# Kernel tuning notes

Hardware: AMD Instinct MI355X
Metric: run time of the kernel (lower is better)

Reference implementation:

```python
import jax, jax.numpy as jnp
import numpy as np
from math import comb

B = 1024                 # num_batch
NUM, NVAR, NUM_OBS = 100, 11, 10
T_FIN = 15.0
K_P = 20.0; K_D = 2.0 * np.sqrt(20.0); K_P_V = 20.0
A_OBS, B_OBS = 8.0, 4.2
RHO_V, RHO_PROJ, RHO_LANE, RHO_OBS, RHO_OFFSET, RHO_INEQ = 1.0, 1.0, 100.0, 100.0, 1.0, 100.0
V_MIN, V_MAX, A_MAX = 0.1, 30.0, 8.0
MAXITER = 20
LATENT, HID, INP_DIM, TRAJ_DIM = 2, 1024, 55, 200


def _bernstein():
    # degree-10 Bernstein polynomial basis on [0, T_FIN], sampled at NUM points
    n = NVAR - 1
    s = np.linspace(0.0, 1.0, NUM)
    bm = lambda m: np.stack([comb(m, k) * s**k * (1.0 - s)**(m - k) for k in range(m + 1)], 1)
    P, B9, B8 = bm(n), bm(n - 1), bm(n - 2)
    Z = np.zeros(NUM)
    Pdot = np.stack([(n / T_FIN) * ((B9[:, k - 1] if k >= 1 else Z) - (B9[:, k] if k <= n - 1 else Z)) for k in range(n + 1)], 1)
    Pddot = np.stack([(n * (n - 1) / T_FIN**2) * ((B8[:, k - 2] if k >= 2 else Z) - 2.0 * (B8[:, k - 1] if 1 <= k <= n - 1 else Z) + (B8[:, k] if k <= n - 2 else Z)) for k in range(n + 1)], 1)
    return tuple(jnp.asarray(a, jnp.float32) for a in (P, Pdot, Pddot))


def _forward(inp, initial_state_ego, traj_gt, y_ub, y_lb, eps,
             enc_w1, enc_b1, enc_w2, enc_b2, enc_wmu, enc_bmu, enc_wlv, enc_blv,
             dec_w1, dec_b1, dec_w2, dec_b2, dec_w3, dec_b3,
             P, Pdot, Pddot, inp_mean, inp_std):
    Bn = inp.shape[0]
    tot_time = jnp.linspace(0.0, T_FIN, NUM)

    # ---- cVAE encode / reparameterize / decode ----
    inp_n = (inp - inp_mean) / inp_std
    h = jax.nn.relu(jnp.concatenate([inp_n, traj_gt], 1) @ enc_w1 + enc_b1)
    h = jax.nn.relu(h @ enc_w2 + enc_b2)
    mu = h @ enc_wmu + enc_bmu
    logvar = h @ enc_wlv + enc_blv
    z = mu + jnp.exp(0.5 * logvar) * eps
    h = jax.nn.relu(jnp.concatenate([z, inp_n], 1) @ dec_w1 + dec_b1)
    h = jax.nn.relu(h @ dec_w2 + dec_b2)
    nn_out = h @ dec_w3 + dec_b3          # (B, 8): 4 v_des + 4 y_des setpoints

    # ---- constant constraint matrices ----
    A_eq_x = jnp.stack([P[0], Pdot[0], Pddot[0]])                 # (3, 11)
    A_eq_y = jnp.stack([P[0], Pdot[0], Pddot[0], Pdot[-1]])       # (4, 11)
    A_pd = Pddot - K_P * P - K_D * Pdot
    A_vd = Pddot - K_P_V * Pdot
    cost_smooth = Pddot.T @ Pddot
    I = jnp.eye(NVAR, dtype=P.dtype)

    def kkt_inv(cost, A_eq):
        m = A_eq.shape[0]
        M = jnp.block([[cost, A_eq.T], [A_eq, jnp.zeros((m, m), cost.dtype)]])
        return jnp.linalg.inv(M)

    # ---- boundary conditions ----
    zb = jnp.zeros((Bn,), inp.dtype)
    b_eq_x = jnp.stack([zb, initial_state_ego[:, 2], zb], 1)
    b_eq_y = jnp.stack([zb, initial_state_ego[:, 3], zb, zb], 1)

    # ---- QP layer 1 (behavioral layer) ----
    # sum_i A_vd_i^T A_vd_i over the 4 row-partitions == A_vd^T A_vd
    cost1_x = cost_smooth + RHO_V * (A_vd.T @ A_vd)
    cost1_y = cost_smooth + RHO_OFFSET * (A_pd.T @ A_pd)
    inv1_x = kkt_inv(cost1_x, A_eq_x)
    inv1_y = kkt_inv(cost1_y, A_eq_y)
    v_des = jnp.repeat(nn_out[:, 0:4], NUM // 4, axis=1)   # (B, 100) piecewise setpoints
    y_des = jnp.repeat(nn_out[:, 4:8], NUM // 4, axis=1)
    lincost_x1 = -RHO_V * ((-K_P_V * v_des) @ A_vd)
    lincost_y1 = -RHO_OFFSET * ((-K_P * y_des) @ A_pd)
    c_x_bar = (jnp.concatenate([-lincost_x1, b_eq_x], 1) @ inv1_x.T)[:, :NVAR]
    c_y_bar = (jnp.concatenate([-lincost_y1, b_eq_y], 1) @ inv1_y.T)[:, :NVAR]

    # ---- obstacle constant-velocity rollouts (obstacle-major, matches tile(P)) ----
    x_obs, y_obs = inp[:, 5::5], inp[:, 6::5]
    vx_obs, vy_obs = inp[:, 7::5], inp[:, 8::5]
    x_obs_traj = (x_obs[:, :, None] + vx_obs[:, :, None] * tot_time).reshape(Bn, NUM_OBS * NUM)
    y_obs_traj = (y_obs[:, :, None] + vy_obs[:, :, None] * tot_time).reshape(Bn, NUM_OBS * NUM)

    # ---- QP layer 2 (iterative ADMM-style projection) ----
    A_obs_m = jnp.tile(P, (NUM_OBS, 1))          # (1000, 11)
    A_lane = jnp.vstack([P, -P])                 # (200, 11)
    A_vel, A_acc = Pdot, Pddot
    cost2_x = RHO_PROJ * I + RHO_OBS * (A_obs_m.T @ A_obs_m) + RHO_INEQ * (A_acc.T @ A_acc) + RHO_INEQ * (A_vel.T @ A_vel)
    cost2_y = cost2_x + RHO_LANE * (A_lane.T @ A_lane)
    inv2_x = kkt_inv(cost2_x, A_eq_x)
    inv2_y = kkt_inv(cost2_y, A_eq_y)
    ones_num = jnp.ones((1, NUM), inp.dtype)
    b_lane = jnp.concatenate([y_ub[:, None] * ones_num, -y_lb[:, None] * ones_num], 1)  # (B, 200)

    def step(carry, _):
        primal, lx, ly = carry
        cx, cy = primal[:, :NVAR], primal[:, NVAR:]
        x, xdot, xddot = cx @ P.T, cx @ Pdot.T, cx @ Pddot.T
        y, ydot, yddot = cy @ P.T, cy @ Pdot.T, cy @ Pddot.T
        # obstacle polar decomposition
        wc = jnp.tile(x, (1, NUM_OBS)) - x_obs_traj
        ws = jnp.tile(y, (1, NUM_OBS)) - y_obs_traj
        a_o = jnp.arctan2(A_OBS * ws, B_OBS * wc)
        ca, sa = jnp.cos(a_o), jnp.sin(a_o)
        c1 = RHO_OBS * (A_OBS**2 * ca**2 + B_OBS**2 * sa**2)
        c2 = RHO_OBS * (A_OBS * wc * ca + B_OBS * ws * sa)
        d_o = jnp.maximum(1.0, c2 / c1)
        # velocity / acceleration polar decomposition with box clipping
        a_v = jnp.arctan2(ydot, xdot)
        cv, sv = jnp.cos(a_v), jnp.sin(a_v)
        d_v = jnp.clip(xdot * cv + ydot * sv, V_MIN, V_MAX)
        a_a = jnp.arctan2(yddot, xddot)
        caa, saa = jnp.cos(a_a), jnp.sin(a_a)
        d_a = jnp.clip(xddot * caa + yddot * saa, 0.0, A_MAX)
        # lane slack
        lane_proj = cy @ A_lane.T
        s_lane = jnp.maximum(0.0, b_lane - lane_proj)
        res_lane = lane_proj - b_lane + s_lane
        # residuals -> dual updates
        rxo = wc - A_OBS * d_o * ca
        ryo = ws - B_OBS * d_o * sa
        rvx, rvy = xdot - d_v * cv, ydot - d_v * sv
        rax, ray = xddot - d_a * caa, yddot - d_a * saa
        lx = lx - RHO_OBS * (rxo @ A_obs_m) - RHO_INEQ * (rax @ A_acc) - RHO_INEQ * (rvx @ A_vel)
        ly = ly - RHO_OBS * (ryo @ A_obs_m) - RHO_INEQ * (ray @ A_acc) - RHO_INEQ * (rvy @ A_vel) - RHO_LANE * (res_lane @ A_lane)
        # linear cost + batched KKT solve via precomputed inverse
        b_ox = x_obs_traj + A_OBS * d_o * ca
        b_oy = y_obs_traj + B_OBS * d_o * sa
        lin_x = -lx - RHO_PROJ * c_x_bar - RHO_OBS * (b_ox @ A_obs_m) - RHO_INEQ * ((d_a * caa) @ A_acc) - RHO_INEQ * ((d_v * cv) @ A_vel)
        lin_y = -ly - RHO_PROJ * c_y_bar - RHO_OBS * (b_oy @ A_obs_m) - RHO_INEQ * ((d_a * saa) @ A_acc) - RHO_INEQ * ((d_v * sv) @ A_vel) - RHO_LANE * ((b_lane - s_lane) @ A_lane)
        sx = (jnp.concatenate([-lin_x, b_eq_x], 1) @ inv2_x.T)[:, :NVAR]
        sy = (jnp.concatenate([-lin_y, b_eq_y], 1) @ inv2_y.T)[:, :NVAR]
        return (jnp.concatenate([sx, sy], 1), lx, ly), None

    primal0 = jnp.concatenate([c_x_bar, c_y_bar], 1)
    lam0 = jnp.zeros((Bn, NVAR), inp.dtype)
    (primal, _, _), _ = jax.lax.scan(step, (primal0, lam0, lam0), None, length=MAXITER)
    return primal  # (B, 2*NVAR) projected trajectory coefficients


def setup_inputs() -> dict:
    key = jax.random.key(0)
    ks = jax.random.split(key, 16)
    P, Pdot, Pddot = _bernstein()
    n = lambda k, sh, sc=1.0: sc * jax.random.normal(k, sh, jnp.float32)
    return {
        "inp": n(ks[0], (B, INP_DIM), 5.0),
        "initial_state_ego": jnp.concatenate([jnp.zeros((B, 2), jnp.float32), 10.0 + n(ks[1], (B, 2))], 1),
        "traj_gt": n(ks[2], (B, TRAJ_DIM)),
        "y_ub": jnp.full((B,), 3.5, jnp.float32),
        "y_lb": jnp.full((B,), -3.5, jnp.float32),
        "eps": n(ks[3], (B, LATENT)),
        "enc_w1": n(ks[4], (INP_DIM + TRAJ_DIM, HID), 0.05), "enc_b1": jnp.zeros((HID,), jnp.float32),
        "enc_w2": n(ks[5], (HID, HID), 0.03), "enc_b2": jnp.zeros((HID,), jnp.float32),
        "enc_wmu": n(ks[6], (HID, LATENT), 0.03), "enc_bmu": jnp.zeros((LATENT,), jnp.float32),
        "enc_wlv": n(ks[7], (HID, LATENT), 0.03), "enc_blv": jnp.zeros((LATENT,), jnp.float32),
        "dec_w1": n(ks[8], (LATENT + INP_DIM, HID), 0.05), "dec_b1": jnp.zeros((HID,), jnp.float32),
        "dec_w2": n(ks[9], (HID, HID), 0.03), "dec_b2": jnp.zeros((HID,), jnp.float32),
        "dec_w3": n(ks[10], (HID, 8), 0.03), "dec_b3": jnp.zeros((8,), jnp.float32),
        "P": P, "Pdot": Pdot, "Pddot": Pddot,
        "inp_mean": jnp.zeros((INP_DIM,), jnp.float32),
        "inp_std": jnp.ones((INP_DIM,), jnp.float32),
    }


def reference(inp, initial_state_ego, traj_gt, y_ub, y_lb, eps,
              enc_w1, enc_b1, enc_w2, enc_b2, enc_wmu, enc_bmu, enc_wlv, enc_blv,
              dec_w1, dec_b1, dec_w2, dec_b2, dec_w3, dec_b3,
              P, Pdot, Pddot, inp_mean, inp_std):
    return _forward(inp, initial_state_ego, traj_gt, y_ub, y_lb, eps,
                    enc_w1, enc_b1, enc_w2, enc_b2, enc_wmu, enc_bmu, enc_wlv, enc_blv,
                    dec_w1, dec_b1, dec_w2, dec_b2, dec_w3, dec_b3,
                    P, Pdot, Pddot, inp_mean, inp_std)
```

## Files before the change

kernel.cpp:

```cpp
#include <hip/hip_runtime.h>
#include <hip/hip_bf16.h>
#include <math.h>

#define BATCH   1024
#define NUMPT   100
#define NVAR    11
#define NOBS    10
#define HID     1024
#define INPD    55
#define TRAJD   200

#define T_FIN_C   15.0f
#define K_P_C     20.0f
#define K_D_C     8.944271909999159f
#define K_P_V_C   20.0f
#define A_OBS_C   8.0f
#define B_OBS_C   4.2f
#define AB_C      33.6f
#define ABSQ_C    1128.96f
#define RHO_V_C      1.0f
#define RHO_PROJ_C   1.0f
#define RHO_LANE_C   100.0f
#define RHO_OBS_C    100.0f
#define RHO_OFFSET_C 1.0f
#define RHO_INEQ_C   100.0f
#define V_MIN_C   0.1f
#define V_MAX_C   30.0f
#define A_MAX_C   8.0f
#define MAXIT     20

#define WS_INV1X  0
#define WS_INV1Y  256
#define WS_INV2X  512
#define WS_INV2Y  768
#define WS_SVD    1024
#define WS_SPD    1088
#define WS_QX     1152
#define WS_QY     1280
#define WS_R2X    1408
#define WS_R2Y    1536
#define WS_BIG    2048

typedef __bf16 bf16x8 __attribute__((ext_vector_type(8)));
typedef float  f32x4  __attribute__((ext_vector_type(4)));

__global__ __launch_bounds__(256) void setup_kernel(
    const float* __restrict__ Pg, const float* __restrict__ Pdg,
    const float* __restrict__ Pddg, float* __restrict__ ws,
    const float* __restrict__ inp, const float* __restrict__ traj,
    const float* __restrict__ mean, const float* __restrict__ stdv,
    __bf16* __restrict__ enc_in, __bf16* __restrict__ dec_in,
    const float* __restrict__ w1, const float* __restrict__ w2,
    const float* __restrict__ w3, const float* __restrict__ w4,
    __bf16* __restrict__ o1, __bf16* __restrict__ o2,
    __bf16* __restrict__ o3, __bf16* __restrict__ o4)
{
    __shared__ float sP[NUMPT*NVAR], sPd[NUMPT*NVAR], sPdd[NUMPT*NVAR];
    __shared__ float aug[15][31];
    __shared__ float fcol[15];
    __shared__ float sQ[121];
    __shared__ float sn[INPD];
    __shared__ float s_pivinv;
    __shared__ int   s_pidx;
    const int tid = threadIdx.x, bid = blockIdx.x;

    if (bid >= 1028) {
        const int idx = (bid - 1028) * 256 + tid;
        if (idx < 262144) {
            const int n = idx >> 8, k = idx & 255;
            o1[idx] = (__bf16)((k < 255) ? w1[(size_t)k*HID + n] : 0.0f);
        } else if (idx < 262144 + 1048576) {
            const int i = idx - 262144;
            const int n = i >> 10, k = i & 1023;
            o2[i] = (__bf16)w2[(size_t)k*HID + n];
        } else if (idx < 262144 + 1048576 + 65536) {
            const int i = idx - (262144 + 1048576);
            const int n = i >> 6, k = i & 63;
            o3[i] = (__bf16)((k < 57) ? w3[(size_t)k*HID + n] : 0.0f);
        } else {
            const int i = idx - (262144 + 1048576 + 65536);
            const int n = i >> 10, k = i & 1023;
            o4[i] = (__bf16)w4[(size_t)k*HID + n];
        }
        return;
    }

    if (bid >= 4) {
        const int b = bid - 4;
        if (tid < INPD) {
            const float v = (inp[b*INPD + tid] - mean[tid]) / stdv[tid];
            sn[tid] = v;
            enc_in[b*256 + tid] = (__bf16)v;
        } else if (tid < 255) {
            enc_in[b*256 + tid] = (__bf16)traj[b*TRAJD + (tid - INPD)];
        } else {
            enc_in[b*256 + 255] = (__bf16)0.0f;
        }
        __syncthreads();
        if (tid >= 2 && tid < 64)
            dec_in[b*64 + tid] = (__bf16)((tid < 57) ? sn[tid - 2] : 0.0f);
        return;
    }

    for (int i = tid; i < NUMPT*NVAR; i += 256) {
        sP[i] = Pg[i]; sPd[i] = Pdg[i]; sPdd[i] = Pddg[i];
    }
    for (int i = tid; i < 15*31; i += 256) (&aug[0][0])[i] = 0.0f;
    __syncthreads();

    const int N = (bid == 0 || bid == 2) ? 14 : 15;

    if (tid < 121) {
        const int i = tid / 11, j = tid % 11;
        float s = 0.0f;
        if (bid == 0) {
            for (int t = 0; t < NUMPT; ++t) {
                float pdd_i = sPdd[t*NVAR+i], pdd_j = sPdd[t*NVAR+j];
                float av_i = pdd_i - K_P_V_C * sPd[t*NVAR+i];
                float av_j = pdd_j - K_P_V_C * sPd[t*NVAR+j];
                s += pdd_i*pdd_j + RHO_V_C * av_i*av_j;
            }
        } else if (bid == 1) {
            for (int t = 0; t < NUMPT; ++t) {
                float pdd_i = sPdd[t*NVAR+i], pdd_j = sPdd[t*NVAR+j];
                float ap_i = pdd_i - K_P_C*sP[t*NVAR+i] - K_D_C*sPd[t*NVAR+i];
                float ap_j = pdd_j - K_P_C*sP[t*NVAR+j] - K_D_C*sPd[t*NVAR+j];
                s += pdd_i*pdd_j + RHO_OFFSET_C * ap_i*ap_j;
            }
        } else {
            float obs_w = RHO_OBS_C * (float)NOBS;
            if (bid == 3) obs_w += RHO_LANE_C * 2.0f;
            for (int t = 0; t < NUMPT; ++t) {
                float p_i = sP[t*NVAR+i],   p_j = sP[t*NVAR+j];
                float pd_i = sPd[t*NVAR+i], pd_j = sPd[t*NVAR+j];
                float pdd_i = sPdd[t*NVAR+i], pdd_j = sPdd[t*NVAR+j];
                s += obs_w*p_i*p_j + RHO_INEQ_C*(pdd_i*pdd_j + pd_i*pd_j);
            }
            if (i == j) s += RHO_PROJ_C;
        }
        aug[i][j] = s;
    }
    if (tid < 11) {
        const int i = tid;
        float a0 = sP[i], a1 = sPd[i], a2 = sPdd[i];
        aug[i][11] = a0; aug[11][i] = a0;
        aug[i][12] = a1; aug[12][i] = a1;
        aug[i][13] = a2; aug[13][i] = a2;
        if (N == 15) { float a3 = sPd[99*NVAR + i]; aug[i][14] = a3; aug[14][i] = a3; }
    }
    if (tid < N) aug[tid][N + tid] = 1.0f;

    if (bid == 0 && tid < 44) {
        const int c = tid / 11, k = tid % 11;
        float sv = 0.0f, sp = 0.0f;
        for (int t = 25*c; t < 25*c + 25; ++t) {
            float p = sP[t*NVAR+k], pd = sPd[t*NVAR+k], pdd = sPdd[t*NVAR+k];
            sv += pdd - K_P_V_C * pd;
            sp += pdd - K_P_C * p - K_D_C * pd;
        }
        ws[WS_SVD + tid] = sv;
        ws[WS_SPD + tid] = sp;
    }
    __syncthreads();

    if ((bid == 2 || bid == 3) && tid < 121) {
        float v = aug[tid/11][tid%11];
        if (tid/11 == tid%11) v -= RHO_PROJ_C;
        sQ[tid] = v;
        ws[(bid == 2 ? WS_QX : WS_QY) + tid] = v;
    }

    for (int k = 0; k < N; ++k) {
        if (tid == 0) {
            int p = k; float best = fabsf(aug[k][k]);
            for (int i = k+1; i < N; ++i) {
                float v = fabsf(aug[i][k]);
                if (v > best) { best = v; p = i; }
            }
            s_pidx = p;
        }
        __syncthreads();
        const int p = s_pidx;
        if (p != k && tid < 2*N) {
            float tmp = aug[k][tid]; aug[k][tid] = aug[p][tid]; aug[p][tid] = tmp;
        }
        __syncthreads();
        if (tid == 0) s_pivinv = 1.0f / aug[k][k];
        __syncthreads();
        if (tid < 2*N) aug[k][tid] *= s_pivinv;
        __syncthreads();
        if (tid < N) fcol[tid] = (tid == k) ? 0.0f : aug[tid][k];
        __syncthreads();
        for (int idx = tid; idx < N*2*N; idx += 256) {
            const int i = idx / (2*N), j = idx % (2*N);
            if (i != k) aug[i][j] = fmaf(-fcol[i], aug[k][j], aug[i][j]);
        }
        __syncthreads();
    }

    float* dst = ws + (bid == 0 ? WS_INV1X : bid == 1 ? WS_INV1Y
                      : bid == 2 ? WS_INV2X : WS_INV2Y);
    for (int idx = tid; idx < N*N; idx += 256)
        dst[idx] = aug[idx / N][N + idx % N];
    __syncthreads();

    if ((bid == 2 || bid == 3) && tid < 121) {
        const int k = tid / 11, j = tid % 11;
        float a = 0.0f;
        #pragma unroll
        for (int m = 0; m < 11; ++m) a = fmaf(aug[k][N + m], sQ[m*11 + j], a);
        ws[(bid == 2 ? WS_R2X : WS_R2Y) + tid] = a;
    }
}

__global__ __launch_bounds__(512) void gemm_mfma(
    const __bf16* __restrict__ A, const __bf16* __restrict__ Wt,
    const float* __restrict__ bias, __bf16* __restrict__ C, int Kp)
{
    __shared__ __bf16 As[64][72];
    __shared__ __bf16 Bs[64][72];
    const int tid = threadIdx.x;
    const int lane = tid & 63, wv = tid >> 6;
    const int wm = (wv >> 1) * 16, wn = (wv & 1) * 32;
    const int ln = lane & 15, q = lane >> 4;
    const int row0 = blockIdx.y * 64, col0 = blockIdx.x * 64;
    const int lrow = tid >> 3, lc = (tid & 7) * 8;

    f32x4 acc0 = (f32x4){0,0,0,0}, acc1 = (f32x4){0,0,0,0};

    for (int k0 = 0; k0 < Kp; k0 += 64) {
        *(bf16x8*)&As[lrow][lc] =
            *(const bf16x8*)&A[(size_t)(row0 + lrow) * Kp + k0 + lc];
        *(bf16x8*)&Bs[lrow][lc] =
            *(const bf16x8*)&Wt[(size_t)(col0 + lrow) * Kp + k0 + lc];
        __syncthreads();
        #pragma unroll
        for (int kc = 0; kc < 2; ++kc) {
            const bf16x8 a  = *(const bf16x8*)&As[wm + ln][kc*32 + q*8];
            const bf16x8 b0 = *(const bf16x8*)&Bs[wn + ln][kc*32 + q*8];
            const bf16x8 b1 = *(const bf16x8*)&Bs[wn + 16 + ln][kc*32 + q*8];
            acc0 = __builtin_amdgcn_mfma_f32_16x16x32_bf16(a, b0, acc0, 0, 0, 0);
            acc1 = __builtin_amdgcn_mfma_f32_16x16x32_bf16(a, b1, acc1, 0, 0, 0);
        }
        __syncthreads();
    }
    #pragma unroll
    for (int ni = 0; ni < 2; ++ni) {
        const int col = col0 + wn + ni*16 + ln;
        const float bv = bias[col];
        const f32x4 av = ni ? acc1 : acc0;
        #pragma unroll
        for (int r = 0; r < 4; ++r) {
            const int row = row0 + wm + q*4 + r;
            C[(size_t)row * HID + col] = (__bf16)fmaxf(av[r] + bv, 0.0f);
        }
    }
}

__global__ __launch_bounds__(64) void z_kernel(
    const __bf16* __restrict__ h, const float* __restrict__ wmu,
    const float* __restrict__ bmu, const float* __restrict__ wlv,
    const float* __restrict__ blv, const float* __restrict__ eps,
    __bf16* __restrict__ dec_in)
{
    const int b = blockIdx.x, lane = threadIdx.x;
    float a0 = 0, a1 = 0, a2 = 0, a3 = 0;
    for (int hh = lane; hh < HID; hh += 64) {
        const float v = (float)h[b*HID + hh];
        a0 = fmaf(v, wmu[hh*2 + 0], a0);
        a1 = fmaf(v, wmu[hh*2 + 1], a1);
        a2 = fmaf(v, wlv[hh*2 + 0], a2);
        a3 = fmaf(v, wlv[hh*2 + 1], a3);
    }
    #pragma unroll
    for (int off = 32; off; off >>= 1) {
        a0 += __shfl_down(a0, off);
        a1 += __shfl_down(a1, off);
        a2 += __shfl_down(a2, off);
        a3 += __shfl_down(a3, off);
    }
    if (lane == 0) {
        const float mu0 = a0 + bmu[0], mu1 = a1 + bmu[1];
        const float lv0 = a2 + blv[0], lv1 = a3 + blv[1];
        dec_in[b*64 + 0] = (__bf16)fmaf(expf(0.5f*lv0), eps[b*2 + 0], mu0);
        dec_in[b*64 + 1] = (__bf16)fmaf(expf(0.5f*lv1), eps[b*2 + 1], mu1);
    }
}

__global__ __launch_bounds__(64) void out8_kernel(
    const __bf16* __restrict__ h, const float* __restrict__ w3,
    const float* __restrict__ b3, float* __restrict__ nn_out)
{
    const int b = blockIdx.x, lane = threadIdx.x;
    float acc[8] = {};
    for (int hh = lane; hh < HID; hh += 64) {
        const float v = (float)h[b*HID + hh];
        #pragma unroll
        for (int j = 0; j < 8; ++j) acc[j] = fmaf(v, w3[hh*8 + j], acc[j]);
    }
    #pragma unroll
    for (int j = 0; j < 8; ++j)
        #pragma unroll
        for (int off = 32; off; off >>= 1) acc[j] += __shfl_down(acc[j], off);
    if (lane == 0)
        for (int j = 0; j < 8; ++j) nn_out[b*8 + j] = acc[j] + b3[j];
}

#define DOT11(bb, a0, a1, a2) \
    fmaf(bb[0],a0.x, fmaf(bb[1],a0.y, fmaf(bb[2],a0.z, fmaf(bb[3],a0.w, \
    fmaf(bb[4],a1.x, fmaf(bb[5],a1.y, fmaf(bb[6],a1.z, fmaf(bb[7],a1.w, \
    fmaf(bb[8],a2.x, fmaf(bb[9],a2.y, bb[10]*a2.z))))))))))

__global__ __launch_bounds__(256) void solver_kernel(
    const float* __restrict__ nn_out, const float* __restrict__ inp,
    const float* __restrict__ ise, const float* __restrict__ yub_p,
    const float* __restrict__ ylb_p,
    const float* __restrict__ Pg, const float* __restrict__ Pdg,
    const float* __restrict__ Pddg,
    const float* __restrict__ ws, float* __restrict__ out)
{
    __shared__ __align__(16) float sBcol[3][11][108];
    __shared__ float s_i2x[196], s_i2y[225], sR2x[121], sR2y[121];
    __shared__ __align__(16) float rows[9][104];
    __shared__ float dval[2][100];
    __shared__ __align__(16) float cxs[12], cys[12];
    __shared__ float wlin[24];
    __shared__ float obsS[4][10];

    const int tid = threadIdx.x;
    const int e = blockIdx.x;

    for (int i = tid; i < 3*11*108; i += 256) {
        const int mat = i / 1188, rem = i - mat*1188;
        const int k = rem / 108, t = rem - k*108;
        const float* G = (mat == 0) ? Pg : (mat == 1 ? Pdg : Pddg);
        sBcol[mat][k][t] = (t < NUMPT) ? G[t*NVAR + k] : 0.0f;
    }
    for (int i = tid; i < 196; i += 256) s_i2x[i] = ws[WS_INV2X + i];
    for (int i = tid; i < 225; i += 256) s_i2y[i] = ws[WS_INV2Y + i];
    for (int i = tid; i < 121; i += 256) { sR2x[i] = ws[WS_R2X + i]; sR2y[i] = ws[WS_R2Y + i]; }
    if (tid >= 200 && tid < 240) {
        const int i = tid - 200;
        obsS[i/10][i%10] = inp[e*INPD + 5 + (i/10) + 5*(i%10)];
    }
    if (tid >= 64 && tid < 100) {
        const int i = tid - 64;
        rows[i >> 2][100 + (i & 3)] = 0.0f;
    }
    if (tid == 100) cxs[11] = 0.0f;
    if (tid == 101) cys[11] = 0.0f;

    const bool isA = (tid < 200);
    const int tA = tid >> 1, hA = tid & 1;
    const bool isB = (tid < 198);
    const int hB = (tid >= 99) ? 1 : 0;
    const int dB = tid - 99*hB;
    const int rB = dB / 11, kB = dB - 11*rB;
    const int mB = (rB==2||rB==6) ? 2 : ((rB==3||rB==7) ? 1 : 0);
    const float* colp = &sBcol[mB][kB][hB*52];
    const float* rowp = &rows[rB][hB*52];

    float bP[NVAR], bPd[NVAR], bPdd[NVAR];
    if (isA) {
        #pragma unroll
        for (int k = 0; k < NVAR; ++k) bP[k] = Pg[tA*NVAR+k];
        if (hA == 0) {
            #pragma unroll
            for (int k = 0; k < NVAR; ++k) {
                bPd[k] = Pdg[tA*NVAR+k]; bPdd[k] = Pddg[tA*NVAR+k];
            }
        }
    }

    const float vx0 = ise[e*4 + 2], vy0 = ise[e*4 + 3];
    const float yub = yub_p[e], ylb = ylb_p[e];
    __syncthreads();

    const float DT = T_FIN_C / 99.0f;
    float xo[5], yo[5];
    if (isA) {
        const int ob0 = 5*hA;
        #pragma unroll
        for (int o = 0; o < 5; ++o) {
            xo[o] = fmaf(obsS[2][ob0+o], tA*DT, obsS[0][ob0+o]);
            yo[o] = fmaf(obsS[3][ob0+o], tA*DT, obsS[1][ob0+o]);
        }
    }

    if (tid < 11) {
        float s = 0;
        #pragma unroll
        for (int c = 0; c < 4; ++c)
            s = fmaf(nn_out[e*8 + c], ws[WS_SVD + c*11 + tid], s);
        wlin[tid] = RHO_V_C * K_P_V_C * s;
    } else if (tid < 22) {
        const int k = tid - 11;
        float s = 0;
        #pragma unroll
        for (int c = 0; c < 4; ++c)
            s = fmaf(nn_out[e*8 + 4 + c], ws[WS_SPD + c*11 + k], s);
        wlin[tid] = RHO_OFFSET_C * K_P_C * s;
    }
    __syncthreads();

    float lam = 0.0f, cb = 0.0f;
    if (tid < 11) {
        const int k = tid;
        float a = vx0 * ws[WS_INV1X + k*14 + 12];
        #pragma unroll
        for (int j = 0; j < NVAR; ++j)
            a = fmaf(-wlin[j], ws[WS_INV1X + k*14 + j], a);
        cb = a; cxs[k] = a;
    } else if (tid < 22) {
        const int k = tid - 11;
        float a = vy0 * ws[WS_INV1Y + k*15 + 12];
        #pragma unroll
        for (int j = 0; j < NVAR; ++j)
            a = fmaf(-wlin[11 + j], ws[WS_INV1Y + k*15 + j], a);
        cb = a; cys[k] = a;
    }
    __syncthreads();

    for (int it = 0; it < MAXIT; ++it) {
        if (isA) {
            const float4 x0 = *(const float4*)&cxs[0];
            const float4 x1 = *(const float4*)&cxs[4];
            const float4 x2 = *(const float4*)&cxs[8];
            const float4 y0 = *(const float4*)&cys[0];
            const float4 y1 = *(const float4*)&cys[4];
            const float4 y2 = *(const float4*)&cys[8];
            const float px = DOT11(bP, x0, x1, x2);
            const float py = DOT11(bP, y0, y1, y2);

            float srx = 0.0f, sry = 0.0f;
            #pragma unroll
            for (int o = 0; o < 5; ++o) {
                const float wc = px - xo[o], wsv = py - yo[o];
                const float aw = A_OBS_C * wsv, bw = B_OBS_C * wc;
                const float r2 = aw*aw + bw*bw;
                if (r2 > 0.0f) {
                    const float f = (r2 < ABSQ_C) ? (1.0f - AB_C * rsqrtf(r2)) : 0.0f;
                    srx = fmaf(wc, f, srx);
                    sry = fmaf(wsv, f, sry);
                } else {
                    srx -= A_OBS_C;
                }
            }
            rows[hA ? 1 : 0][tA] = srx;
            rows[hA ? 5 : 4][tA] = sry;

            if (hA == 0) {
                const float pxd  = DOT11(bPd,  x0, x1, x2);
                const float pyd  = DOT11(bPd,  y0, y1, y2);
                const float pxdd = DOT11(bPdd, x0, x1, x2);
                const float pydd = DOT11(bPdd, y0, y1, y2);
                const float rv2 = pxd*pxd + pyd*pyd;
                float vxr, vyr;
                if (rv2 > 0.0f) {
                    const float ri = rsqrtf(rv2);
                    const float dv = fminf(fmaxf(rv2*ri, V_MIN_C), V_MAX_C);
                    const float f = 1.0f - dv*ri;
                    vxr = pxd*f; vyr = pyd*f;
                } else { vxr = -V_MIN_C; vyr = 0.0f; }
                rows[3][tA] = vxr;  rows[7][tA] = vyr;
                const float ra2 = pxdd*pxdd + pydd*pydd;
                float axr = 0.0f, ayr = 0.0f;
                if (ra2 > ABSQ_C*0.0f + A_MAX_C*A_MAX_C) {
                    const float ri = rsqrtf(ra2);
                    const float f = 1.0f - A_MAX_C*ri;
                    axr = pxdd*f; ayr = pydd*f;
                }
                rows[2][tA] = axr;  rows[6][tA] = ayr;
                rows[8][tA] = fmaxf(0.0f, py - yub) - fmaxf(0.0f, ylb - py);
            }
        }
        __syncthreads();

        if (isB) {
            float s = 0.0f;
            #pragma unroll
            for (int i = 0; i < 13; ++i) {
                const float4 rr = *(const float4*)&rowp[i*4];
                const float4 cc = *(const float4*)&colp[i*4];
                s = fmaf(rr.x, cc.x, s); s = fmaf(rr.y, cc.y, s);
                s = fmaf(rr.z, cc.z, s); s = fmaf(rr.w, cc.w, s);
            }
            dval[hB][dB] = s;
        }
        __syncthreads();

        if (tid < 22) {
            const int k = (tid < 11) ? tid : tid - 11;
            float u;
            if (tid < 11)
                u = RHO_OBS_C * ((dval[0][k]      + dval[1][k])
                               + (dval[0][11 + k] + dval[1][11 + k])
                               + (dval[0][22 + k] + dval[1][22 + k])
                               + (dval[0][33 + k] + dval[1][33 + k]));
            else
                u = RHO_OBS_C * ((dval[0][44 + k] + dval[1][44 + k])
                               + (dval[0][55 + k] + dval[1][55 + k])
                               + (dval[0][66 + k] + dval[1][66 + k])
                               + (dval[0][77 + k] + dval[1][77 + k])
                               + (dval[0][88 + k] + dval[1][88 + k]));
            wlin[tid] = 2.0f*u - lam - cb;
            lam -= u;
        }
        __builtin_amdgcn_wave_barrier();
        if (tid < 22) {
            const int k = (tid < 11) ? tid : tid - 11;
            if (tid < 11) {
                float a = vx0 * s_i2x[k*14 + 12];
                #pragma unroll
                for (int j = 0; j < NVAR; ++j) {
                    a = fmaf(-wlin[j], s_i2x[k*14 + j], a);
                    a = fmaf(sR2x[k*11 + j], cxs[j], a);
                }
                cxs[k] = a;
            } else {
                float a = vy0 * s_i2y[k*15 + 12];
                #pragma unroll
                for (int j = 0; j < NVAR; ++j) {
                    a = fmaf(-wlin[11 + j], s_i2y[k*15 + j], a);
                    a = fmaf(sR2y[k*11 + j], cys[j], a);
                }
                cys[k] = a;
            }
        }
        __syncthreads();
    }

    if (tid < NVAR) {
        out[e*22 + tid]      = cxs[tid];
        out[e*22 + 11 + tid] = cys[tid];
    }
}

extern "C" void kernel_launch(void* const* d_in, const int* in_sizes, int n_in,
                              void* d_out, int out_size, void* d_ws, size_t ws_size,
                              hipStream_t stream)
{
    (void)in_sizes; (void)n_in; (void)out_size; (void)ws_size;
    const float* inp    = (const float*)d_in[0];
    const float* ise    = (const float*)d_in[1];
    const float* traj   = (const float*)d_in[2];
    const float* yub    = (const float*)d_in[3];
    const float* ylb    = (const float*)d_in[4];
    const float* eps    = (const float*)d_in[5];
    const float* enc_w1 = (const float*)d_in[6];
    const float* enc_b1 = (const float*)d_in[7];
    const float* enc_w2 = (const float*)d_in[8];
    const float* enc_b2 = (const float*)d_in[9];
    const float* wmu    = (const float*)d_in[10];
    const float* bmu    = (const float*)d_in[11];
    const float* wlv    = (const float*)d_in[12];
    const float* blv    = (const float*)d_in[13];
    const float* dec_w1 = (const float*)d_in[14];
    const float* dec_b1 = (const float*)d_in[15];
    const float* dec_w2 = (const float*)d_in[16];
    const float* dec_b2 = (const float*)d_in[17];
    const float* dec_w3 = (const float*)d_in[18];
    const float* dec_b3 = (const float*)d_in[19];
    const float* P      = (const float*)d_in[20];
    const float* Pd     = (const float*)d_in[21];
    const float* Pdd    = (const float*)d_in[22];
    const float* mean   = (const float*)d_in[23];
    const float* stdv   = (const float*)d_in[24];

    float* ws   = (float*)d_ws;
    float* nn   = ws + WS_BIG;
    __bf16* bfb = (__bf16*)(ws + WS_BIG + BATCH*8);
    __bf16* enc_in = bfb;
    __bf16* dec_in = enc_in + (size_t)BATCH*256;
    __bf16* hA     = dec_in + (size_t)BATCH*64;
    __bf16* hB     = hA + (size_t)BATCH*HID;
    __bf16* wt1    = hB + (size_t)BATCH*HID;
    __bf16* wt2    = wt1 + (size_t)HID*256;
    __bf16* wt3    = wt2 + (size_t)HID*HID;
    __bf16* wt4    = wt3 + (size_t)HID*64;
    float* outf = (float*)d_out;

    setup_kernel<<<4 + 1024 + 9472, 256, 0, stream>>>(
        P, Pd, Pdd, ws, inp, traj, mean, stdv, enc_in, dec_in,
        enc_w1, enc_w2, dec_w1, dec_w2, wt1, wt2, wt3, wt4);

    dim3 g(16, 16);
    gemm_mfma<<<g, 512, 0, stream>>>(enc_in, wt1, enc_b1, hA, 256);
    gemm_mfma<<<g, 512, 0, stream>>>(hA, wt2, enc_b2, hB, 1024);
    z_kernel<<<BATCH, 64, 0, stream>>>(hB, wmu, bmu, wlv, blv, eps, dec_in);
    gemm_mfma<<<g, 512, 0, stream>>>(dec_in, wt3, dec_b1, hA, 64);
    gemm_mfma<<<g, 512, 0, stream>>>(hA, wt4, dec_b2, hB, 1024);
    out8_kernel<<<BATCH, 64, 0, stream>>>(hB, dec_w3, dec_b3, nn);

    solver_kernel<<<BATCH, 256, 0, stream>>>(nn, inp, ise, yub, ylb,
                                             P, Pd, Pdd, ws, outf);
}
```

Before: 264.3 us.

## Shrink GEMM tiles to 32x64 and rebalance solver thread work

```diff
diff --git a/kernel.cpp b/kernel.cpp
--- a/kernel.cpp
+++ b/kernel.cpp
@@ -213,26 +213,28 @@
     }
 }
 
-__global__ __launch_bounds__(512) void gemm_mfma(
+__global__ __launch_bounds__(256) void gemm_mfma(
     const __bf16* __restrict__ A, const __bf16* __restrict__ Wt,
     const float* __restrict__ bias, __bf16* __restrict__ C, int Kp)
 {
-    __shared__ __bf16 As[64][72];
+    __shared__ __bf16 As[32][72];
     __shared__ __bf16 Bs[64][72];
     const int tid = threadIdx.x;
     const int lane = tid & 63, wv = tid >> 6;
     const int wm = (wv >> 1) * 16, wn = (wv & 1) * 32;
     const int ln = lane & 15, q = lane >> 4;
-    const int row0 = blockIdx.y * 64, col0 = blockIdx.x * 64;
-    const int lrow = tid >> 3, lc = (tid & 7) * 8;
+    const int row0 = blockIdx.y * 32, col0 = blockIdx.x * 64;
+    const int srow = tid >> 3, lc = (tid & 7) * 8;
 
     f32x4 acc0 = (f32x4){0,0,0,0}, acc1 = (f32x4){0,0,0,0};
 
     for (int k0 = 0; k0 < Kp; k0 += 64) {
-        *(bf16x8*)&As[lrow][lc] =
-            *(const bf16x8*)&A[(size_t)(row0 + lrow) * Kp + k0 + lc];
-        *(bf16x8*)&Bs[lrow][lc] =
-            *(const bf16x8*)&Wt[(size_t)(col0 + lrow) * Kp + k0 + lc];
+        *(bf16x8*)&As[srow][lc] =
+            *(const bf16x8*)&A[(size_t)(row0 + srow) * Kp + k0 + lc];
+        *(bf16x8*)&Bs[srow][lc] =
+            *(const bf16x8*)&Wt[(size_t)(col0 + srow) * Kp + k0 + lc];
+        *(bf16x8*)&Bs[srow + 32][lc] =
+            *(const bf16x8*)&Wt[(size_t)(col0 + srow + 32) * Kp + k0 + lc];
         __syncthreads();
         #pragma unroll
         for (int kc = 0; kc < 2; ++kc) {
@@ -321,8 +323,8 @@
 {
     __shared__ __align__(16) float sBcol[3][11][108];
     __shared__ float s_i2x[196], s_i2y[225], sR2x[121], sR2y[121];
-    __shared__ __align__(16) float rows[9][104];
-    __shared__ float dval[2][100];
+    __shared__ __align__(16) float rows[7][104];
+    __shared__ float dval[2][80];
     __shared__ __align__(16) float cxs[12], cys[12];
     __shared__ float wlin[24];
     __shared__ float obsS[4][10];
@@ -343,32 +345,30 @@
         const int i = tid - 200;
         obsS[i/10][i%10] = inp[e*INPD + 5 + (i/10) + 5*(i%10)];
     }
-    if (tid >= 64 && tid < 100) {
+    if (tid >= 64 && tid < 92) {
         const int i = tid - 64;
         rows[i >> 2][100 + (i & 3)] = 0.0f;
     }
-    if (tid == 100) cxs[11] = 0.0f;
-    if (tid == 101) cys[11] = 0.0f;
+    if (tid == 92) cxs[11] = 0.0f;
+    if (tid == 93) cys[11] = 0.0f;
 
     const bool isA = (tid < 200);
     const int tA = tid >> 1, hA = tid & 1;
-    const bool isB = (tid < 198);
-    const int hB = (tid >= 99) ? 1 : 0;
-    const int dB = tid - 99*hB;
+    const bool isB = (tid < 154);
+    const int hB = (tid >= 77) ? 1 : 0;
+    const int dB = tid - 77*hB;
     const int rB = dB / 11, kB = dB - 11*rB;
-    const int mB = (rB==2||rB==6) ? 2 : ((rB==3||rB==7) ? 1 : 0);
+    const int mB = (rB==1||rB==4) ? 2 : ((rB==2||rB==5) ? 1 : 0);
     const float* colp = &sBcol[mB][kB][hB*52];
     const float* rowp = &rows[rB][hB*52];
 
-    float bP[NVAR], bPd[NVAR], bPdd[NVAR];
+    float bP[NVAR], bQ[NVAR];
     if (isA) {
-        #pragma unroll
-        for (int k = 0; k < NVAR; ++k) bP[k] = Pg[tA*NVAR+k];
-        if (hA == 0) {
-            #pragma unroll
-            for (int k = 0; k < NVAR; ++k) {
-                bPd[k] = Pdg[tA*NVAR+k]; bPdd[k] = Pddg[tA*NVAR+k];
-            }
+        const float* Qsrc = hA ? Pddg : Pdg;
+        #pragma unroll
+        for (int k = 0; k < NVAR; ++k) {
+            bP[k] = Pg[tA*NVAR+k];
+            bQ[k] = Qsrc[tA*NVAR+k];
         }
     }
 
@@ -431,6 +431,8 @@
             const float4 y2 = *(const float4*)&cys[8];
             const float px = DOT11(bP, x0, x1, x2);
             const float py = DOT11(bP, y0, y1, y2);
+            const float qx = DOT11(bQ, x0, x1, x2);
+            const float qy = DOT11(bQ, y0, y1, y2);
 
             float srx = 0.0f, sry = 0.0f;
             #pragma unroll
@@ -446,46 +448,45 @@
                     srx -= A_OBS_C;
                 }
             }
-            rows[hA ? 1 : 0][tA] = srx;
-            rows[hA ? 5 : 4][tA] = sry;
+            const float mrx = srx + __shfl_xor(srx, 1);
+            const float mry = sry + __shfl_xor(sry, 1);
 
             if (hA == 0) {
-                const float pxd  = DOT11(bPd,  x0, x1, x2);
-                const float pyd  = DOT11(bPd,  y0, y1, y2);
-                const float pxdd = DOT11(bPdd, x0, x1, x2);
-                const float pydd = DOT11(bPdd, y0, y1, y2);
-                const float rv2 = pxd*pxd + pyd*pyd;
+                rows[0][tA] = mrx;
+                rows[3][tA] = mry;
+                const float rv2 = qx*qx + qy*qy;
                 float vxr, vyr;
                 if (rv2 > 0.0f) {
                     const float ri = rsqrtf(rv2);
                     const float dv = fminf(fmaxf(rv2*ri, V_MIN_C), V_MAX_C);
                     const float f = 1.0f - dv*ri;
-                    vxr = pxd*f; vyr = pyd*f;
+                    vxr = qx*f; vyr = qy*f;
                 } else { vxr = -V_MIN_C; vyr = 0.0f; }
-                rows[3][tA] = vxr;  rows[7][tA] = vyr;
-                const float ra2 = pxdd*pxdd + pydd*pydd;
+                rows[2][tA] = vxr;  rows[5][tA] = vyr;
+                rows[6][tA] = fmaxf(0.0f, py - yub) - fmaxf(0.0f, ylb - py);
+            } else {
+                const float ra2 = qx*qx + qy*qy;
                 float axr = 0.0f, ayr = 0.0f;
-                if (ra2 > ABSQ_C*0.0f + A_MAX_C*A_MAX_C) {
+                if (ra2 > A_MAX_C*A_MAX_C) {
                     const float ri = rsqrtf(ra2);
                     const float f = 1.0f - A_MAX_C*ri;
-                    axr = pxdd*f; ayr = pydd*f;
+                    axr = qx*f; ayr = qy*f;
                 }
-                rows[2][tA] = axr;  rows[6][tA] = ayr;
-                rows[8][tA] = fmaxf(0.0f, py - yub) - fmaxf(0.0f, ylb - py);
+                rows[1][tA] = axr;  rows[4][tA] = ayr;
             }
         }
         __syncthreads();
 
         if (isB) {
-            float s = 0.0f;
+            float s0 = 0.0f, s1 = 0.0f;
             #pragma unroll
             for (int i = 0; i < 13; ++i) {
                 const float4 rr = *(const float4*)&rowp[i*4];
                 const float4 cc = *(const float4*)&colp[i*4];
-                s = fmaf(rr.x, cc.x, s); s = fmaf(rr.y, cc.y, s);
-                s = fmaf(rr.z, cc.z, s); s = fmaf(rr.w, cc.w, s);
-            }
-            dval[hB][dB] = s;
+                s0 = fmaf(rr.x, cc.x, s0); s1 = fmaf(rr.y, cc.y, s1);
+                s0 = fmaf(rr.z, cc.z, s0); s1 = fmaf(rr.w, cc.w, s1);
+            }
+            dval[hB][dB] = s0 + s1;
         }
         __syncthreads();
 
@@ -495,14 +496,12 @@
             if (tid < 11)
                 u = RHO_OBS_C * ((dval[0][k]      + dval[1][k])
                                + (dval[0][11 + k] + dval[1][11 + k])
-                               + (dval[0][22 + k] + dval[1][22 + k])
-                               + (dval[0][33 + k] + dval[1][33 + k]));
+                               + (dval[0][22 + k] + dval[1][22 + k]));
             else
-                u = RHO_OBS_C * ((dval[0][44 + k] + dval[1][44 + k])
+                u = RHO_OBS_C * ((dval[0][33 + k] + dval[1][33 + k])
+                               + (dval[0][44 + k] + dval[1][44 + k])
                                + (dval[0][55 + k] + dval[1][55 + k])
-                               + (dval[0][66 + k] + dval[1][66 + k])
-                               + (dval[0][77 + k] + dval[1][77 + k])
-                               + (dval[0][88 + k] + dval[1][88 + k]));
+                               + (dval[0][66 + k] + dval[1][66 + k]));
             wlin[tid] = 2.0f*u - lam - cb;
             lam -= u;
         }
@@ -584,12 +583,12 @@
         P, Pd, Pdd, ws, inp, traj, mean, stdv, enc_in, dec_in,
         enc_w1, enc_w2, dec_w1, dec_w2, wt1, wt2, wt3, wt4);
 
-    dim3 g(16, 16);
-    gemm_mfma<<<g, 512, 0, stream>>>(enc_in, wt1, enc_b1, hA, 256);
-    gemm_mfma<<<g, 512, 0, stream>>>(hA, wt2, enc_b2, hB, 1024);
+    dim3 g(16, 32);
+    gemm_mfma<<<g, 256, 0, stream>>>(enc_in, wt1, enc_b1, hA, 256);
+    gemm_mfma<<<g, 256, 0, stream>>>(hA, wt2, enc_b2, hB, 1024);
     z_kernel<<<BATCH, 64, 0, stream>>>(hB, wmu, bmu, wlv, blv, eps, dec_in);
-    gemm_mfma<<<g, 512, 0, stream>>>(dec_in, wt3, dec_b1, hA, 64);
-    gemm_mfma<<<g, 512, 0, stream>>>(hA, wt4, dec_b2, hB, 1024);
+    gemm_mfma<<<g, 256, 0, stream>>>(dec_in, wt3, dec_b1, hA, 64);
+    gemm_mfma<<<g, 256, 0, stream>>>(hA, wt4, dec_b2, hB, 1024);
     out8_kernel<<<BATCH, 64, 0, stream>>>(hB, dec_w3, dec_b3, nn);
 
     solver_kernel<<<BATCH, 256, 0, stream>>>(nn, inp, ise, yub, ylb,
```

Result: faster. 236.6 us (-10.5%).
